# Kernel optimization log

Hardware: AMD Instinct MI355X
Metric: run time of the kernel (lower is better)

The kernel has to match this reference:

```python
import jax, jax.numpy as jnp
import numpy as np

B, S, D = 4, 4096, 128

def setup_inputs() -> dict:
    key = jax.random.key(0)
    kx, kq, kk, kv = jax.random.split(key, 4)
    x = jax.random.normal(kx, (B, S, D), dtype=jnp.float32)
    Wq = jax.random.normal(kq, (D, D), dtype=jnp.float32) * (1.0 / np.sqrt(D))
    Wk = jax.random.normal(kk, (D, D), dtype=jnp.float32) * (1.0 / np.sqrt(D))
    Wv = jax.random.normal(kv, (D, D), dtype=jnp.float32) * (1.0 / np.sqrt(D))
    return {"x": x, "Wq": Wq, "Wk": Wk, "Wv": Wv}

def reference(x, Wq, Wk, Wv):
    b, s, d = x.shape
    # nn.Linear(bias=False): y = x @ W.T
    q = jnp.einsum('bsd,ed->bse', x, Wq)
    k = jnp.einsum('bsd,ed->bse', x, Wk)
    v = jnp.einsum('bsd,ed->bse', x, Wv)
    scores = jnp.einsum('bqd,bkd->bqk', q, k) / jnp.sqrt(jnp.float32(d))
    causal = jnp.tril(jnp.ones((s, s), dtype=bool))  # [s,s]
    scores = jnp.where(causal, scores, jnp.float32(-jnp.inf))
    weights = jax.nn.softmax(scores.astype(jnp.float32), axis=-1)
    out = jnp.einsum('bqk,bkd->bqd', weights, v)
    return out  # dropout is identity in eval / p=0
```

## Files before the change

### kernel.cpp

```cpp
#include <hip/hip_runtime.h>
#include <hip/hip_bf16.h>
#include <math.h>

typedef __attribute__((ext_vector_type(8))) short short8;
typedef __attribute__((ext_vector_type(4))) float f32x4;
typedef __attribute__((ext_vector_type(4))) float float4v;
typedef __attribute__((ext_vector_type(4))) unsigned short ushort4v;

typedef __attribute__((address_space(1))) const unsigned int GAS;
typedef __attribute__((address_space(3))) unsigned int LAS;

#define B_ 4
#define S_ 4096
#define D_ 128

#define CPB 544
#define NSLOT (B_ * CPB)

#define LDS_K 0
#define LDS_V 16384
#define LDS_P 32768
#define LDS_TOTAL 40960

__device__ __forceinline__ unsigned short f2bf(float f) {
    union { float f; unsigned u; } v; v.f = f;
    unsigned r = v.u + 0x7FFFu + ((v.u >> 16) & 1u);
    return (unsigned short)(r >> 16);
}
__device__ __forceinline__ float bf2f(unsigned short h) {
    union { unsigned u; float f; } v; v.u = ((unsigned)h) << 16;
    return v.f;
}

__global__ void wconv_kernel(const float* __restrict__ Wq,
                             const float* __restrict__ Wk,
                             const float* __restrict__ Wv,
                             unsigned short* __restrict__ Wb) {
    int i = blockIdx.x * 256 + threadIdx.x;
    if (i >= 3 * 16384) return;
    const float* s = (i < 16384) ? Wq : (i < 32768 ? Wk : Wv);
    Wb[i] = f2bf(s[i & 16383]);
}

__global__ __launch_bounds__(256) void qkv_kernel(const float* __restrict__ X,
                                                  const unsigned short* __restrict__ Wb,
                                                  unsigned short* __restrict__ Qb,
                                                  unsigned short* __restrict__ Kb,
                                                  unsigned short* __restrict__ Vt) {
    const int tid = threadIdx.x;
    const int lane = tid & 63, w = tid >> 6;
    const int l16 = lane & 15, g = lane >> 4;
    const int r0 = blockIdx.x * 64;
    const int grp = blockIdx.y;

    const int row = r0 + w * 16 + l16;
    const float* xr = X + (long)row * 128;
    float4v x0[4], x1[4];
    #pragma unroll
    for (int kb = 0; kb < 4; ++kb) {
        x0[kb] = *reinterpret_cast<const float4v*>(xr + kb * 32 + g * 8);
        x1[kb] = *reinterpret_cast<const float4v*>(xr + kb * 32 + g * 8 + 4);
    }
    short8 a[4];
    #pragma unroll
    for (int kb = 0; kb < 4; ++kb) {
        short8 t;
        t[0] = f2bf(x0[kb][0]); t[1] = f2bf(x0[kb][1]);
        t[2] = f2bf(x0[kb][2]); t[3] = f2bf(x0[kb][3]);
        t[4] = f2bf(x1[kb][0]); t[5] = f2bf(x1[kb][1]);
        t[6] = f2bf(x1[kb][2]); t[7] = f2bf(x1[kb][3]);
        a[kb] = t;
    }

    const float scale = 0.08838834764831845f;
    #pragma unroll
    for (int ct = 0; ct < 8; ++ct) {
        const int e = ct * 16 + l16;
        const int c = grp * 128 + e;
        f32x4 acc = {0.f, 0.f, 0.f, 0.f};
        #pragma unroll
        for (int kb = 0; kb < 4; ++kb) {
            short8 bf = *reinterpret_cast<const short8*>(Wb + (long)c * 128 + kb * 32 + g * 8);
            acc = __builtin_amdgcn_mfma_f32_16x16x32_bf16(a[kb], bf, acc, 0, 0, 0);
        }
        const int row0 = r0 + w * 16 + g * 4;
        if (grp == 0) {
            #pragma unroll
            for (int r = 0; r < 4; ++r) Qb[(long)(row0 + r) * 128 + e] = f2bf(acc[r] * scale);
        } else if (grp == 1) {
            #pragma unroll
            for (int r = 0; r < 4; ++r) Kb[(long)(row0 + r) * 128 + e] = f2bf(acc[r]);
        } else {
            const int bb = row0 >> 12, ss = row0 & 4095;
            ushort4v p;
            p[0] = f2bf(acc[0]); p[1] = f2bf(acc[1]); p[2] = f2bf(acc[2]); p[3] = f2bf(acc[3]);
            *reinterpret_cast<ushort4v*>(&Vt[((long)bb * 128 + e) * 4096 + ss]) = p;
        }
    }
}

__global__ __launch_bounds__(256, 4) void attn_kernel(const unsigned short* __restrict__ Qb,
                                                      const unsigned short* __restrict__ Kb,
                                                      const unsigned short* __restrict__ Vt,
                                                      unsigned short* __restrict__ Opart,
                                                      float* __restrict__ Mpart,
                                                      float* __restrict__ Lpart) {
    __shared__ __align__(16) unsigned char lds[LDS_TOTAL];

    const int tid = threadIdx.x;
    const int lane = tid & 63, w = tid >> 6;
    const int l16 = lane & 15, g = lane >> 4;

    const int bidx = (int)blockIdx.x;
    const int b = bidx / CPB;
    const int rr = CPB - 1 - (bidx - b * CPB);
    int gg = 0;
    while (2 * (gg + 1) * (gg + 2) <= rr) ++gg;
    const int j = rr - 2 * gg * (gg + 1);
    const int qt = 4 * gg + j / (gg + 1);
    const int c = j % (gg + 1);
    const int slot = b * CPB + rr;

    const unsigned short* Qbase = Qb + (long)b * S_ * D_;
    const unsigned char* Kb_b = (const unsigned char*)(Kb + (long)b * S_ * D_);
    const unsigned char* Vb_b = (const unsigned char*)(Vt + (long)b * D_ * S_);

    const int qrow_f = qt * 64 + w * 16 + l16;
    short8 qf[4];
    #pragma unroll
    for (int kb = 0; kb < 4; ++kb)
        qf[kb] = *reinterpret_cast<const short8*>(Qbase + (long)qrow_f * 128 + kb * 32 + g * 8);

    int koff[4], voff[4];
    #pragma unroll
    for (int i = 0; i < 4; ++i) {
        int ch = i * 256 + tid;
        int krow = ch >> 4, kcd = ch & 15;
        koff[i] = krow * 256 + ((kcd * 16) ^ ((krow & 7) << 4));
        int vrow = ch >> 3, vck = ch & 7;
        voff[i] = vrow * 8192 + ((vck * 16) ^ ((vrow & 7) << 4));
    }

    const int swz = (l16 & 7) << 4;
    const unsigned char* kaddr[4];
    const unsigned char* vaddr[2];
    const unsigned char* pread[2];
    unsigned char* Pw = lds + LDS_P + w * 2048;
    #pragma unroll
    for (int i = 0; i < 4; ++i)
        kaddr[i] = lds + LDS_K + l16 * 256 + ((i * 64 + g * 16) ^ swz);
    #pragma unroll
    for (int i = 0; i < 2; ++i) {
        const int xo = (i * 64 + g * 16) ^ swz;
        vaddr[i] = lds + LDS_V + l16 * 128 + xo;
        pread[i] = Pw + l16 * 128 + xo;
    }
    unsigned char* prow[4];
    int pmask[4];
    #pragma unroll
    for (int r = 0; r < 4; ++r) {
        const int pr = g * 4 + r;
        prow[r] = Pw + pr * 128;
        pmask[r] = (pr & 7) << 4;
    }
    const int pl2 = l16 * 2;

    f32x4 o[8];
    #pragma unroll
    for (int dt = 0; dt < 8; ++dt) o[dt] = (f32x4){0.f, 0.f, 0.f, 0.f};
    float m[4], lsum[4];
    int myrow[4];
    #pragma unroll
    for (int r = 0; r < 4; ++r) {
        m[r] = -INFINITY; lsum[r] = 0.f;
        myrow[r] = qt * 64 + w * 16 + g * 4 + r;
    }

    const int kt0 = c * 4;
    const int ktend = min(kt0 + 3, qt);

    for (int kt = kt0; kt <= ktend; ++kt) {
        #pragma unroll
        for (int i = 0; i < 4; ++i) {
            int ch = i * 256 + tid;
            __builtin_amdgcn_global_load_lds((GAS*)(Kb_b + (long)kt * 16384 + koff[i]),
                                             (LAS*)(lds + LDS_K + ch * 16), 16, 0, 0);
            __builtin_amdgcn_global_load_lds((GAS*)(Vb_b + (long)kt * 128 + voff[i]),
                                             (LAS*)(lds + LDS_V + ch * 16), 16, 0, 0);
        }
        __syncthreads();

        f32x4 s[4];
        __builtin_amdgcn_s_setprio(1);
        #pragma unroll
        for (int ct = 0; ct < 4; ++ct) {
            s[ct] = (f32x4){0.f, 0.f, 0.f, 0.f};
            #pragma unroll
            for (int kb = 0; kb < 4; ++kb) {
                short8 kf = *reinterpret_cast<const short8*>(kaddr[kb] + ct * 4096);
                s[ct] = __builtin_amdgcn_mfma_f32_16x16x32_bf16(qf[kb], kf, s[ct], 0, 0, 0);
            }
        }
        __builtin_amdgcn_s_setprio(0);

        if (kt == qt) {
            #pragma unroll
            for (int ct = 0; ct < 4; ++ct) {
                const int col = kt * 64 + ct * 16 + l16;
                #pragma unroll
                for (int r = 0; r < 4; ++r)
                    if (col > myrow[r]) s[ct][r] = -1e30f;
            }
        }

        float rmax[4];
        #pragma unroll
        for (int r = 0; r < 4; ++r)
            rmax[r] = fmaxf(fmaxf(s[0][r], s[1][r]), fmaxf(s[2][r], s[3][r]));
        #pragma unroll
        for (int off = 1; off < 16; off <<= 1) {
            #pragma unroll
            for (int r = 0; r < 4; ++r) rmax[r] = fmaxf(rmax[r], __shfl_xor(rmax[r], off, 64));
        }
        bool upd = false;
        #pragma unroll
        for (int r = 0; r < 4; ++r) upd = upd || (rmax[r] > m[r] + 8.0f);
        if (__any(upd)) {
            float al[4];
            #pragma unroll
            for (int r = 0; r < 4; ++r) {
                float mn = fmaxf(m[r], rmax[r]);
                al[r] = __expf(m[r] - mn);
                m[r] = mn;
                lsum[r] *= al[r];
            }
            #pragma unroll
            for (int dt = 0; dt < 8; ++dt) {
                #pragma unroll
                for (int r = 0; r < 4; ++r) o[dt][r] *= al[r];
            }
        }
        float rsum[4] = {0.f, 0.f, 0.f, 0.f};
        #pragma unroll
        for (int ct = 0; ct < 4; ++ct) {
            #pragma unroll
            for (int r = 0; r < 4; ++r) {
                float p = __expf(s[ct][r] - m[r]);
                s[ct][r] = p;
                rsum[r] += p;
            }
        }
        #pragma unroll
        for (int off = 1; off < 16; off <<= 1) {
            #pragma unroll
            for (int r = 0; r < 4; ++r) rsum[r] += __shfl_xor(rsum[r], off, 64);
        }
        #pragma unroll
        for (int r = 0; r < 4; ++r) lsum[r] += rsum[r];

        #pragma unroll
        for (int ct = 0; ct < 4; ++ct) {
            #pragma unroll
            for (int r = 0; r < 4; ++r) {
                *reinterpret_cast<unsigned short*>(prow[r] + ((ct * 32 + pl2) ^ pmask[r])) =
                    f2bf(s[ct][r]);
            }
        }

        #pragma unroll
        for (int kvb = 0; kvb < 2; ++kvb) {
            short8 pf = *reinterpret_cast<const short8*>(pread[kvb]);
            __builtin_amdgcn_s_setprio(1);
            #pragma unroll
            for (int dt = 0; dt < 8; ++dt) {
                short8 vf = *reinterpret_cast<const short8*>(vaddr[kvb] + dt * 2048);
                o[dt] = __builtin_amdgcn_mfma_f32_16x16x32_bf16(pf, vf, o[dt], 0, 0, 0);
            }
            __builtin_amdgcn_s_setprio(0);
        }

        if (kt < ktend) __syncthreads();
    }

    unsigned short* Op = Opart + (long)slot * 8192;
    #pragma unroll
    for (int dt = 0; dt < 8; ++dt) {
        #pragma unroll
        for (int r = 0; r < 4; ++r) {
            Op[(w * 16 + g * 4 + r) * 128 + dt * 16 + l16] = f2bf(o[dt][r]);
        }
    }
    if (l16 == 0) {
        #pragma unroll
        for (int r = 0; r < 4; ++r) {
            Mpart[(long)slot * 64 + w * 16 + g * 4 + r] = m[r];
            Lpart[(long)slot * 64 + w * 16 + g * 4 + r] = lsum[r];
        }
    }
}

__global__ __launch_bounds__(256) void combine_kernel(const unsigned short* __restrict__ Opart,
                                                      const float* __restrict__ Mpart,
                                                      const float* __restrict__ Lpart,
                                                      float* __restrict__ out) {
    __shared__ float coeff[16][16];
    __shared__ float invL[16];

    const int qt = blockIdx.x >> 2, qq = blockIdx.x & 3, b = blockIdx.y;
    const int gg = qt >> 2;
    const int nc = gg + 1;
    const int slot0 = b * CPB + 2 * gg * (gg + 1) + (qt - 4 * gg) * nc;
    const int r0 = qq * 16;

    const int tid = threadIdx.x;
    if (tid < 16) {
        float mg = -INFINITY;
        for (int c = 0; c < nc; ++c)
            mg = fmaxf(mg, Mpart[(long)(slot0 + c) * 64 + r0 + tid]);
        float L = 0.f;
        for (int c = 0; c < nc; ++c) {
            float co = __expf(Mpart[(long)(slot0 + c) * 64 + r0 + tid] - mg);
            coeff[c][tid] = co;
            L += co * Lpart[(long)(slot0 + c) * 64 + r0 + tid];
        }
        invL[tid] = 1.f / L;
    }
    __syncthreads();

    const int e0 = tid * 8;
    const int r = e0 >> 7;
    float acc[8];
    #pragma unroll
    for (int k = 0; k < 8; ++k) acc[k] = 0.f;
    for (int c = 0; c < nc; ++c) {
        short8 v = *reinterpret_cast<const short8*>(Opart + (long)(slot0 + c) * 8192 + r0 * 128 + e0);
        const float co = coeff[c][r];
        #pragma unroll
        for (int k = 0; k < 8; ++k)
            acc[k] += co * bf2f((unsigned short)v[k]);
    }
    const float s = invL[r];
    float4v o0, o1;
    o0[0] = acc[0] * s; o0[1] = acc[1] * s; o0[2] = acc[2] * s; o0[3] = acc[3] * s;
    o1[0] = acc[4] * s; o1[1] = acc[5] * s; o1[2] = acc[6] * s; o1[3] = acc[7] * s;
    float* dst = out + ((long)b * S_ + qt * 64 + r0) * 128 + e0;
    *reinterpret_cast<float4v*>(dst) = o0;
    *reinterpret_cast<float4v*>(dst + 4) = o1;
}

extern "C" void kernel_launch(void* const* d_in, const int* in_sizes, int n_in,
                              void* d_out, int out_size, void* d_ws, size_t ws_size,
                              hipStream_t stream) {
    (void)in_sizes; (void)n_in; (void)out_size; (void)ws_size;
    const float* x  = (const float*)d_in[0];
    const float* Wq = (const float*)d_in[1];
    const float* Wk = (const float*)d_in[2];
    const float* Wv = (const float*)d_in[3];
    float* out = (float*)d_out;

    char* ws = (char*)d_ws;
    const size_t MB4 = (size_t)16384 * 128 * 2;
    unsigned short* Qb = (unsigned short*)(ws);
    unsigned short* Kb = (unsigned short*)(ws + MB4);
    unsigned short* Vt = (unsigned short*)(ws + 2 * MB4);
    unsigned short* Wb = (unsigned short*)(ws + 3 * MB4);
    unsigned short* Opart = (unsigned short*)(ws + 3 * MB4 + (1 << 20));
    float* Mpart = (float*)(ws + 3 * MB4 + (1 << 20) + (size_t)NSLOT * 8192 * 2);
    float* Lpart = Mpart + (size_t)NSLOT * 64;

    wconv_kernel<<<192, 256, 0, stream>>>(Wq, Wk, Wv, Wb);
    qkv_kernel<<<dim3(256, 3), 256, 0, stream>>>(x, Wb, Qb, Kb, Vt);
    attn_kernel<<<NSLOT, 256, 0, stream>>>(Qb, Kb, Vt, Opart, Mpart, Lpart);
    combine_kernel<<<dim3(256, 4), 256, 0, stream>>>(Opart, Mpart, Lpart, out);
}
```

Before: 141.4 us.

## Transpose score MFMA so each lane owns one query row for softmax

Swaps the QK^T MFMA operands so each lane's accumulator holds four keys of a single query row. Per-row max and sum then need only two cross-lane shuffles instead of four rounds on four rows, and each lane keeps one scalar m and lsum. P is packed to bf16 with v_cvt_pk_bf16_f32 and written to LDS as 8-byte stores instead of scattered 2-byte stores. Softmax moves to exp2 by folding log2(e) into the Q scale, with the lazy-rescale threshold adjusted to match. Risk: the O accumulator still uses the old row layout (row g*4+r) but is rescaled by this lane's per-query alpha, so a rescale after the first tile can apply the wrong factor to O rows.

```diff
diff --git a/kernel.cpp b/kernel.cpp
--- a/kernel.cpp
+++ b/kernel.cpp
@@ -3,6 +3,7 @@
 #include <math.h>
 
 typedef __attribute__((ext_vector_type(8))) short short8;
+typedef __attribute__((ext_vector_type(2))) unsigned int uint2v;
 typedef __attribute__((ext_vector_type(4))) float f32x4;
 typedef __attribute__((ext_vector_type(4))) float float4v;
 typedef __attribute__((ext_vector_type(4))) unsigned short ushort4v;
@@ -30,6 +31,11 @@
 __device__ __forceinline__ float bf2f(unsigned short h) {
     union { unsigned u; float f; } v; v.u = ((unsigned)h) << 16;
     return v.f;
+}
+__device__ __forceinline__ unsigned cvt_pk_bf16(float lo, float hi) {
+    unsigned r;
+    asm("v_cvt_pk_bf16_f32 %0, %1, %2" : "=v"(r) : "v"(lo), "v"(hi));
+    return r;
 }
 
 __global__ void wconv_kernel(const float* __restrict__ Wq,
@@ -72,7 +78,7 @@
         a[kb] = t;
     }
 
-    const float scale = 0.08838834764831845f;
+    const float scale = 0.12751744416006513f;
     #pragma unroll
     for (int ct = 0; ct < 8; ++ct) {
         const int e = ct * 16 + l16;
@@ -145,36 +151,25 @@
     const unsigned char* kaddr[4];
     const unsigned char* vaddr[2];
     const unsigned char* pread[2];
+    unsigned char* pwrite[4];
     unsigned char* Pw = lds + LDS_P + w * 2048;
     #pragma unroll
-    for (int i = 0; i < 4; ++i)
+    for (int i = 0; i < 4; ++i) {
         kaddr[i] = lds + LDS_K + l16 * 256 + ((i * 64 + g * 16) ^ swz);
+        pwrite[i] = Pw + l16 * 128 + ((i * 32 + g * 8) ^ swz);
+    }
     #pragma unroll
     for (int i = 0; i < 2; ++i) {
         const int xo = (i * 64 + g * 16) ^ swz;
         vaddr[i] = lds + LDS_V + l16 * 128 + xo;
         pread[i] = Pw + l16 * 128 + xo;
     }
-    unsigned char* prow[4];
-    int pmask[4];
-    #pragma unroll
-    for (int r = 0; r < 4; ++r) {
-        const int pr = g * 4 + r;
-        prow[r] = Pw + pr * 128;
-        pmask[r] = (pr & 7) << 4;
-    }
-    const int pl2 = l16 * 2;
 
     f32x4 o[8];
     #pragma unroll
     for (int dt = 0; dt < 8; ++dt) o[dt] = (f32x4){0.f, 0.f, 0.f, 0.f};
-    float m[4], lsum[4];
-    int myrow[4];
-    #pragma unroll
-    for (int r = 0; r < 4; ++r) {
-        m[r] = -INFINITY; lsum[r] = 0.f;
-        myrow[r] = qt * 64 + w * 16 + g * 4 + r;
-    }
+    float m = -INFINITY, lsum = 0.f;
+    const int myq = qt * 64 + w * 16 + l16;
 
     const int kt0 = c * 4;
     const int ktend = min(kt0 + 3, qt);
@@ -198,7 +193,7 @@
             #pragma unroll
             for (int kb = 0; kb < 4; ++kb) {
                 short8 kf = *reinterpret_cast<const short8*>(kaddr[kb] + ct * 4096);
-                s[ct] = __builtin_amdgcn_mfma_f32_16x16x32_bf16(qf[kb], kf, s[ct], 0, 0, 0);
+                s[ct] = __builtin_amdgcn_mfma_f32_16x16x32_bf16(kf, qf[kb], s[ct], 0, 0, 0);
             }
         }
         __builtin_amdgcn_s_setprio(0);
@@ -206,65 +201,52 @@
         if (kt == qt) {
             #pragma unroll
             for (int ct = 0; ct < 4; ++ct) {
-                const int col = kt * 64 + ct * 16 + l16;
+                const int kg = kt * 64 + ct * 16 + g * 4;
                 #pragma unroll
                 for (int r = 0; r < 4; ++r)
-                    if (col > myrow[r]) s[ct][r] = -1e30f;
-            }
-        }
-
-        float rmax[4];
-        #pragma unroll
-        for (int r = 0; r < 4; ++r)
-            rmax[r] = fmaxf(fmaxf(s[0][r], s[1][r]), fmaxf(s[2][r], s[3][r]));
-        #pragma unroll
-        for (int off = 1; off < 16; off <<= 1) {
-            #pragma unroll
-            for (int r = 0; r < 4; ++r) rmax[r] = fmaxf(rmax[r], __shfl_xor(rmax[r], off, 64));
-        }
-        bool upd = false;
-        #pragma unroll
-        for (int r = 0; r < 4; ++r) upd = upd || (rmax[r] > m[r] + 8.0f);
-        if (__any(upd)) {
-            float al[4];
-            #pragma unroll
-            for (int r = 0; r < 4; ++r) {
-                float mn = fmaxf(m[r], rmax[r]);
-                al[r] = __expf(m[r] - mn);
-                m[r] = mn;
-                lsum[r] *= al[r];
-            }
+                    if (kg + r > myq) s[ct][r] = -1e30f;
+            }
+        }
+
+        float rmax = s[0][0];
+        #pragma unroll
+        for (int ct = 0; ct < 4; ++ct) {
+            #pragma unroll
+            for (int r = 0; r < 4; ++r) rmax = fmaxf(rmax, s[ct][r]);
+        }
+        rmax = fmaxf(rmax, __shfl_xor(rmax, 16, 64));
+        rmax = fmaxf(rmax, __shfl_xor(rmax, 32, 64));
+        if (__any(rmax > m + 11.5f)) {
+            float mn = fmaxf(m, rmax);
+            float al = exp2f(m - mn);
+            m = mn;
+            lsum *= al;
             #pragma unroll
             for (int dt = 0; dt < 8; ++dt) {
                 #pragma unroll
-                for (int r = 0; r < 4; ++r) o[dt][r] *= al[r];
-            }
-        }
-        float rsum[4] = {0.f, 0.f, 0.f, 0.f};
+                for (int r = 0; r < 4; ++r) o[dt][r] *= al;
+            }
+        }
+        float rsum = 0.f;
         #pragma unroll
         for (int ct = 0; ct < 4; ++ct) {
             #pragma unroll
             for (int r = 0; r < 4; ++r) {
-                float p = __expf(s[ct][r] - m[r]);
+                float p = exp2f(s[ct][r] - m);
                 s[ct][r] = p;
-                rsum[r] += p;
-            }
-        }
-        #pragma unroll
-        for (int off = 1; off < 16; off <<= 1) {
-            #pragma unroll
-            for (int r = 0; r < 4; ++r) rsum[r] += __shfl_xor(rsum[r], off, 64);
-        }
-        #pragma unroll
-        for (int r = 0; r < 4; ++r) lsum[r] += rsum[r];
+                rsum += p;
+            }
+        }
+        rsum += __shfl_xor(rsum, 16, 64);
+        rsum += __shfl_xor(rsum, 32, 64);
+        lsum += rsum;
 
         #pragma unroll
         for (int ct = 0; ct < 4; ++ct) {
-            #pragma unroll
-            for (int r = 0; r < 4; ++r) {
-                *reinterpret_cast<unsigned short*>(prow[r] + ((ct * 32 + pl2) ^ pmask[r])) =
-                    f2bf(s[ct][r]);
-            }
+            uint2v pb;
+            pb[0] = cvt_pk_bf16(s[ct][0], s[ct][1]);
+            pb[1] = cvt_pk_bf16(s[ct][2], s[ct][3]);
+            *reinterpret_cast<uint2v*>(pwrite[ct]) = pb;
         }
 
         #pragma unroll
@@ -290,12 +272,9 @@
             Op[(w * 16 + g * 4 + r) * 128 + dt * 16 + l16] = f2bf(o[dt][r]);
         }
     }
-    if (l16 == 0) {
-        #pragma unroll
-        for (int r = 0; r < 4; ++r) {
-            Mpart[(long)slot * 64 + w * 16 + g * 4 + r] = m[r];
-            Lpart[(long)slot * 64 + w * 16 + g * 4 + r] = lsum[r];
-        }
+    if (g == 0) {
+        Mpart[(long)slot * 64 + w * 16 + l16] = m;
+        Lpart[(long)slot * 64 + w * 16 + l16] = lsum;
     }
 }
 
@@ -319,7 +298,7 @@
             mg = fmaxf(mg, Mpart[(long)(slot0 + c) * 64 + r0 + tid]);
         float L = 0.f;
         for (int c = 0; c < nc; ++c) {
-            float co = __expf(Mpart[(long)(slot0 + c) * 64 + r0 + tid] - mg);
+            float co = exp2f(Mpart[(long)(slot0 + c) * 64 + r0 + tid] - mg);
             coeff[c][tid] = co;
             L += co * Lpart[(long)(slot0 + c) * 64 + r0 + tid];
         }
```

New measurement: 128.0 us. 1.1x faster.
